# Optimization experiments

Measured on AMD Instinct MI355X. Metric: run time of the kernel, lower is better.

The kernel has to match this reference:

```python
import jax, jax.numpy as jnp
import numpy as np

B, T, C = 4, 2048, 1024
H = 16
D = C // H  # head_dim = 64


def setup_inputs() -> dict:
    key = jax.random.key(0)
    k1, k2, k3, k4, k5 = jax.random.split(key, 5)
    s = 0.02
    return {
        "x": jax.random.normal(k1, (B, T, C), dtype=jnp.float32),
        "W_qkv": jax.random.normal(k2, (C, 3 * C), dtype=jnp.float32) * s,
        "b_qkv": jax.random.normal(k3, (3 * C,), dtype=jnp.float32) * s,
        "W_o": jax.random.normal(k4, (C, C), dtype=jnp.float32) * s,
        "b_o": jax.random.normal(k5, (C,), dtype=jnp.float32) * s,
    }


def reference(x, W_qkv, b_qkv, W_o, b_o):
    b, t, c = x.shape
    scaling = D ** (-0.5)
    qkv = x @ W_qkv + b_qkv                      # [B,T,3C]
    q, k, v = jnp.split(qkv, 3, axis=-1)         # each [B,T,C]
    q = q.reshape(b, t, H, D).transpose(0, 2, 1, 3)  # [B,H,T,D]
    k = k.reshape(b, t, H, D).transpose(0, 2, 1, 3)
    v = v.reshape(b, t, H, D).transpose(0, 2, 1, 3)
    scores = jnp.einsum("bhqd,bhkd->bhqk", q, k) * scaling  # [B,H,T,T]
    mask = jnp.tril(jnp.ones((t, t), dtype=bool))            # causal
    scores = jnp.where(mask[None, None, :, :], scores, -jnp.inf)
    probs = jax.nn.softmax(scores, axis=-1)
    out = jnp.einsum("bhqk,bhkd->bhqd", probs, v)            # [B,H,T,D]
    out = out.transpose(0, 2, 1, 3).reshape(b, t, c)         # [B,T,C]
    return out @ W_o + b_o
```

## Files before the change

kernel.cpp:

```cpp
#include <hip/hip_runtime.h>
#include <hip/hip_bf16.h>

typedef unsigned short ushort_t;
typedef __attribute__((ext_vector_type(8))) short short8;
typedef __attribute__((ext_vector_type(4))) float floatx4;
typedef __attribute__((ext_vector_type(2))) unsigned uint2v;
typedef __attribute__((ext_vector_type(4))) unsigned uint4v;

#define B_ 4
#define T_ 2048
#define C_ 1024
#define H_ 16
#define D_ 64
#define BT_ (B_ * T_)
#define N3C (3 * C_)

#define KSC 0.18033688011112042f

__device__ __forceinline__ ushort_t f2bf(float f) {
    unsigned u = __float_as_uint(f);
    u += 0x7FFF + ((u >> 16) & 1);
    return (ushort_t)(u >> 16);
}
__device__ __forceinline__ unsigned pack2bf(float a, float b) {
    __hip_bfloat162 h = __float22bfloat162_rn(make_float2(a, b));
    return *(unsigned*)&h;
}

__device__ __forceinline__ void gload16(const ushort_t* g, ushort_t* l) {
    __builtin_amdgcn_global_load_lds((const __attribute__((address_space(1))) void*)g,
                                     (__attribute__((address_space(3))) void*)l, 16, 0, 0);
}

__global__ void convert_x_k(const float* __restrict__ xin, ushort_t* __restrict__ xb) {
    size_t i = ((size_t)blockIdx.x * 256 + threadIdx.x) * 8;
    const float* xf = xin + i;
    float4 a = *(const float4*)xf;
    float4 b = *(const float4*)(xf + 4);
    short8 o;
    o[0] = (short)f2bf(a.x); o[1] = (short)f2bf(a.y);
    o[2] = (short)f2bf(a.z); o[3] = (short)f2bf(a.w);
    o[4] = (short)f2bf(b.x); o[5] = (short)f2bf(b.y);
    o[6] = (short)f2bf(b.z); o[7] = (short)f2bf(b.w);
    *(short8*)&xb[i] = o;
}

__global__ void transpose_k(const float* __restrict__ in, ushort_t* __restrict__ out,
                            int R, int Nc) {
    __shared__ ushort_t t[32][33];
    int bc = blockIdx.x * 32;
    int br = blockIdx.y * 32;
    int lx = threadIdx.x & 31, ly = threadIdx.x >> 5;
#pragma unroll
    for (int i = 0; i < 4; ++i) {
        int r = ly + i * 8;
        t[r][lx] = f2bf(in[(size_t)(br + r) * Nc + bc + lx]);
    }
    __syncthreads();
#pragma unroll
    for (int i = 0; i < 4; ++i) {
        int r = ly + i * 8;
        out[(size_t)(bc + r) * R + br + lx] = t[lx][r];
    }
}

__global__ void vtrans_k(const ushort_t* __restrict__ in, ushort_t* __restrict__ out) {
    __shared__ ushort_t t[32][33];
    int bh = blockIdx.z;
    const ushort_t* I = in + (size_t)bh * T_ * D_;
    ushort_t* O = out + (size_t)bh * D_ * T_;
    int bt = blockIdx.x * 32, bd = blockIdx.y * 32;
    int lx = threadIdx.x & 31, ly = threadIdx.x >> 5;
#pragma unroll
    for (int i = 0; i < 4; ++i) {
        int r = ly + i * 8;
        t[r][lx] = I[(size_t)(bt + r) * D_ + bd + lx];
    }
    __syncthreads();
#pragma unroll
    for (int i = 0; i < 4; ++i) {
        int r = ly + i * 8;
        O[(size_t)(bd + r) * T_ + bt + lx] = t[lx][r];
    }
}

template <int MODE>
__launch_bounds__(256)
__global__ void gemm_bt(const ushort_t* __restrict__ A, const ushort_t* __restrict__ Bt,
                        const float* __restrict__ bias, float* __restrict__ Cout,
                        ushort_t* __restrict__ Qo, ushort_t* __restrict__ Ko,
                        ushort_t* __restrict__ Vo, int M, int N, int K) {
    __shared__ __align__(16) ushort_t Alds[128 * 32];
    __shared__ __align__(16) ushort_t Blds[128 * 32];
    int tid = threadIdx.x;
    int wave = tid >> 6, lane = tid & 63;
    int bm = blockIdx.x * 128, bn = blockIdx.y * 128;
    int wr = (wave >> 1) * 64, wc = (wave & 1) * 64;
    int lm = lane & 15, lk = (lane >> 4) * 8, lq = lane >> 4;

    floatx4 acc[4][4] = {};

    int srow = tid >> 2;
    int scol = (tid & 3) * 8;
    const ushort_t* Ab = A + (size_t)(bm + srow) * K + scol;
    const ushort_t* Bb = Bt + (size_t)(bn + srow) * K + scol;
    ushort_t* Al0 = &Alds[wave * 512];
    ushort_t* Al1 = &Alds[2048 + wave * 512];
    ushort_t* Bl0 = &Blds[wave * 512];
    ushort_t* Bl1 = &Blds[2048 + wave * 512];
    size_t rowskip = (size_t)64 * K;

    for (int k0 = 0; k0 < K; k0 += 32) {
        __syncthreads();
        gload16(Ab + k0, Al0);
        gload16(Ab + k0 + rowskip, Al1);
        gload16(Bb + k0, Bl0);
        gload16(Bb + k0 + rowskip, Bl1);
        __syncthreads();
        short8 af[4], bf[4];
#pragma unroll
        for (int i = 0; i < 4; ++i)
            af[i] = *(const short8*)&Alds[(wr + i * 16 + lm) * 32 + lk];
#pragma unroll
        for (int i = 0; i < 4; ++i)
            bf[i] = *(const short8*)&Blds[(wc + i * 16 + lm) * 32 + lk];
#pragma unroll
        for (int mi = 0; mi < 4; ++mi)
#pragma unroll
            for (int ni = 0; ni < 4; ++ni)
                acc[mi][ni] = __builtin_amdgcn_mfma_f32_16x16x32_bf16(
                    af[mi], bf[ni], acc[mi][ni], 0, 0, 0);
    }

#pragma unroll
    for (int mi = 0; mi < 4; ++mi) {
#pragma unroll
        for (int ni = 0; ni < 4; ++ni) {
            int col = bn + wc + ni * 16 + lm;
            float bv = bias[col];
#pragma unroll
            for (int r = 0; r < 4; ++r) {
                int row = bm + wr + mi * 16 + lq * 4 + r;
                float v = acc[mi][ni][r] + bv;
                if (MODE == 0) {
                    Cout[(size_t)row * N + col] = v;
                } else {
                    int b = row >> 11, t = row & (T_ - 1);
                    int which = col >> 10, c = col & (C_ - 1);
                    int h = c >> 6, d = c & 63;
                    int bh = b * H_ + h;
                    size_t idx = ((size_t)bh * T_ + t) * D_ + d;
                    if (which == 0)
                        Qo[idx] = f2bf(v * KSC);
                    else if (which == 1)
                        Ko[idx] = f2bf(v);
                    else
                        Vo[idx] = f2bf(v);
                }
            }
        }
    }
}

__launch_bounds__(256)
__global__ void attn_k(const ushort_t* __restrict__ Q, const ushort_t* __restrict__ K,
                       const ushort_t* __restrict__ Vt, ushort_t* __restrict__ O) {
    __shared__ __align__(16) ushort_t Klds[64 * 72];
    __shared__ __align__(16) ushort_t Vlds[64 * 72];

    int tid = threadIdx.x, wave = tid >> 6, lane = tid & 63;
    int id = blockIdx.x;
    int xcd = id & 7, j = id >> 3;
    int band = 31 - (j & 31);
    int bh = xcd + 8 * (j >> 5);
    int b = bh >> 4, h = bh & 15;
    int lm = lane & 15, lq = lane >> 4;

    const ushort_t* Qp = Q + (size_t)bh * T_ * D_;
    const ushort_t* Kp = K + (size_t)bh * T_ * D_;
    const ushort_t* Vp = Vt + (size_t)bh * D_ * T_;
    ushort_t* Ob = O + ((size_t)b * T_) * C_ + h * D_;

    int srow = tid >> 2, scol = (tid & 3) * 16;
    const ushort_t* Kg = Kp + (size_t)srow * D_ + scol;
    const ushort_t* Vg = Vp + (size_t)srow * T_ + scol;
    ushort_t* Kl = &Klds[srow * 72 + scol];
    ushort_t* Vl = &Vlds[srow * 72 + scol];

    short8 onesf = {};
    if (lm == 0) {
#pragma unroll
        for (int jj = 0; jj < 8; ++jj) onesf[jj] = (short)0x3F80;
    }

    int m0 = band * 64 + wave * 16;

    short8 qf0 = *(const short8*)&Qp[(size_t)(m0 + lm) * D_ + lq * 8];
    short8 qf1 = *(const short8*)&Qp[(size_t)(m0 + lm) * D_ + 32 + lq * 8];

    floatx4 oacc[5] = {};

    int ntw = band + 1;
    short8 kr0 = *(const short8*)Kg;
    short8 kr1 = *(const short8*)(Kg + 8);
    short8 vr0 = *(const short8*)Vg;
    short8 vr1 = *(const short8*)(Vg + 8);

    for (int it = 0; it < ntw; ++it) {
        __syncthreads();
        *(short8*)Kl = kr0;
        *(short8*)(Kl + 8) = kr1;
        *(short8*)Vl = vr0;
        *(short8*)(Vl + 8) = vr1;
        __syncthreads();

        if (it + 1 < ntw) {
            const ushort_t* kn = Kg + (size_t)(it + 1) * 64 * D_;
            const ushort_t* vn = Vg + (it + 1) * 64;
            kr0 = *(const short8*)kn;
            kr1 = *(const short8*)(kn + 8);
            vr0 = *(const short8*)vn;
            vr1 = *(const short8*)(vn + 8);
        }

        short8 kf[4][2], vf[4][2];
#pragma unroll
        for (int nt = 0; nt < 4; ++nt) {
            kf[nt][0] = *(const short8*)&Klds[(nt * 16 + lm) * 72 + lq * 8];
            kf[nt][1] = *(const short8*)&Klds[(nt * 16 + lm) * 72 + 32 + lq * 8];
        }

        floatx4 st[4] = {};
#pragma unroll
        for (int nt = 0; nt < 4; ++nt) {
            st[nt] = __builtin_amdgcn_mfma_f32_16x16x32_bf16(kf[nt][0], qf0, st[nt], 0, 0, 0);
            st[nt] = __builtin_amdgcn_mfma_f32_16x16x32_bf16(kf[nt][1], qf1, st[nt], 0, 0, 0);
        }

#pragma unroll
        for (int dt = 0; dt < 4; ++dt) {
            vf[dt][0] = *(const short8*)&Vlds[(dt * 16 + lm) * 72 + lq * 8];
            vf[dt][1] = *(const short8*)&Vlds[(dt * 16 + lm) * 72 + 32 + lq * 8];
        }

        int kv0 = it * 64;
        if (it == ntw - 1) {
            int mg = m0 + lm;
#pragma unroll
            for (int nt = 0; nt < 4; ++nt)
#pragma unroll
                for (int r = 0; r < 4; ++r) {
                    int kvg = kv0 + nt * 16 + lq * 4 + r;
                    if (kvg > mg) st[nt][r] = -__builtin_inff();
                }
        }

        unsigned e0 = pack2bf(exp2f(st[0][0]), exp2f(st[0][1]));
        unsigned e1 = pack2bf(exp2f(st[0][2]), exp2f(st[0][3]));
        unsigned e2 = pack2bf(exp2f(st[1][0]), exp2f(st[1][1]));
        unsigned e3 = pack2bf(exp2f(st[1][2]), exp2f(st[1][3]));
        unsigned e4 = pack2bf(exp2f(st[2][0]), exp2f(st[2][1]));
        unsigned e5 = pack2bf(exp2f(st[2][2]), exp2f(st[2][3]));
        unsigned e6 = pack2bf(exp2f(st[3][0]), exp2f(st[3][1]));
        unsigned e7 = pack2bf(exp2f(st[3][2]), exp2f(st[3][3]));

        uint2v ra = __builtin_amdgcn_permlane32_swap(e0, e2, false, false);
        uint2v wa = __builtin_amdgcn_permlane16_swap(ra[0], ra[1], false, false);
        uint2v rb = __builtin_amdgcn_permlane32_swap(e1, e3, false, false);
        uint2v wb = __builtin_amdgcn_permlane16_swap(rb[0], rb[1], false, false);
        uint2v rc = __builtin_amdgcn_permlane32_swap(e4, e6, false, false);
        uint2v wc = __builtin_amdgcn_permlane16_swap(rc[0], rc[1], false, false);
        uint2v rd = __builtin_amdgcn_permlane32_swap(e5, e7, false, false);
        uint2v wd = __builtin_amdgcn_permlane16_swap(rd[0], rd[1], false, false);

        short8 pb0 = __builtin_bit_cast(short8, (uint4v){wa[0], wb[0], wa[1], wb[1]});
        short8 pb1 = __builtin_bit_cast(short8, (uint4v){wc[0], wd[0], wc[1], wd[1]});

#pragma unroll
        for (int dt = 0; dt < 4; ++dt) {
            oacc[dt] = __builtin_amdgcn_mfma_f32_16x16x32_bf16(vf[dt][0], pb0, oacc[dt], 0, 0, 0);
            oacc[dt] = __builtin_amdgcn_mfma_f32_16x16x32_bf16(vf[dt][1], pb1, oacc[dt], 0, 0, 0);
        }
        oacc[4] = __builtin_amdgcn_mfma_f32_16x16x32_bf16(onesf, pb0, oacc[4], 0, 0, 0);
        oacc[4] = __builtin_amdgcn_mfma_f32_16x16x32_bf16(onesf, pb1, oacc[4], 0, 0, 0);
    }

    float li = __shfl(oacc[4][0], lm, 64);
    float inv = 1.0f / li;
    int tg = m0 + lm;
#pragma unroll
    for (int dt = 0; dt < 4; ++dt) {
        uint2 pk;
        pk.x = pack2bf(oacc[dt][0] * inv, oacc[dt][1] * inv);
        pk.y = pack2bf(oacc[dt][2] * inv, oacc[dt][3] * inv);
        *(uint2*)&Ob[(size_t)tg * C_ + dt * 16 + lq * 4] = pk;
    }
}

extern "C" void kernel_launch(void* const* d_in, const int* in_sizes, int n_in,
                              void* d_out, int out_size, void* d_ws, size_t ws_size,
                              hipStream_t stream) {
    const float* x    = (const float*)d_in[0];
    const float* Wqkv = (const float*)d_in[1];
    const float* bqkv = (const float*)d_in[2];
    const float* Wo   = (const float*)d_in[3];
    const float* bo   = (const float*)d_in[4];

    ushort_t* ws = (ushort_t*)d_ws;
    ushort_t* WqkvT = ws;
    ushort_t* WoT   = WqkvT + (size_t)N3C * C_;
    ushort_t* Xb    = WoT + (size_t)C_ * C_;
    ushort_t* Qs    = Xb + (size_t)BT_ * C_;
    ushort_t* Ks    = Qs + (size_t)BT_ * C_;
    ushort_t* Vs    = Ks + (size_t)BT_ * C_;
    ushort_t* Attn  = Vs + (size_t)BT_ * C_;

    convert_x_k<<<BT_ * C_ / (256 * 8), 256, 0, stream>>>(x, Xb);
    transpose_k<<<dim3(N3C / 32, C_ / 32), 256, 0, stream>>>(Wqkv, WqkvT, C_, N3C);
    transpose_k<<<dim3(C_ / 32, C_ / 32), 256, 0, stream>>>(Wo, WoT, C_, C_);
    gemm_bt<1><<<dim3(BT_ / 128, N3C / 128), 256, 0, stream>>>(
        Xb, WqkvT, bqkv, nullptr, Qs, Ks, Attn, BT_, N3C, C_);
    vtrans_k<<<dim3(T_ / 32, D_ / 32, B_ * H_), 256, 0, stream>>>(Attn, Vs);
    attn_k<<<2048, 256, 0, stream>>>(Qs, Ks, Vs, Attn);
    gemm_bt<0><<<dim3(BT_ / 128, C_ / 128), 256, 0, stream>>>(
        Attn, WoT, bo, (float*)d_out, nullptr, nullptr, nullptr, BT_, C_, C_);
}
```

Measured before the change: 290.4 us.

## Double-buffer K/V tiles in LDS with direct global-to-LDS loads and XOR swizzle

The attention kernel now stages K and V tiles through a two-slot LDS buffer filled by direct global-to-LDS loads (gload16), replacing the register-staged copy. The padded 72-stride layout becomes an XOR-swizzled 64-stride layout to avoid bank conflicts. This removes one of the two barriers per iteration and the register round-trip. It also swaps exp2f for the raw hardware exp2 builtin, which drops the range handling the library call performs. It relies on gload16 being defined elsewhere and doubles the LDS footprint.

```diff
diff --git a/kernel.cpp b/kernel.cpp
--- a/kernel.cpp
+++ b/kernel.cpp
@@ -165,8 +165,7 @@
 __launch_bounds__(256)
 __global__ void attn_k(const ushort_t* __restrict__ Q, const ushort_t* __restrict__ K,
                        const ushort_t* __restrict__ Vt, ushort_t* __restrict__ O) {
-    __shared__ __align__(16) ushort_t Klds[64 * 72];
-    __shared__ __align__(16) ushort_t Vlds[64 * 72];
+    __shared__ __align__(16) ushort_t KV[2][2][64 * 64];
 
     int tid = threadIdx.x, wave = tid >> 6, lane = tid & 63;
     int id = blockIdx.x;
@@ -174,18 +173,19 @@
     int band = 31 - (j & 31);
     int bh = xcd + 8 * (j >> 5);
     int b = bh >> 4, h = bh & 15;
-    int lm = lane & 15, lq = lane >> 4;
+    int lm = lane & 15, lq = lane >> 4, m7 = lane & 7;
 
     const ushort_t* Qp = Q + (size_t)bh * T_ * D_;
     const ushort_t* Kp = K + (size_t)bh * T_ * D_;
     const ushort_t* Vp = Vt + (size_t)bh * D_ * T_;
     ushort_t* Ob = O + ((size_t)b * T_) * C_ + h * D_;
 
-    int srow = tid >> 2, scol = (tid & 3) * 16;
-    const ushort_t* Kg = Kp + (size_t)srow * D_ + scol;
-    const ushort_t* Vg = Vp + (size_t)srow * T_ + scol;
-    ushort_t* Kl = &Klds[srow * 72 + scol];
-    ushort_t* Vl = &Vlds[srow * 72 + scol];
+    int sr = lane >> 3;
+    int sc = (lane & 7) ^ sr;
+    const ushort_t* Kst = Kp + (size_t)(wave * 16 + sr) * D_ + sc * 8;
+    const ushort_t* Vst = Vp + (size_t)(wave * 16 + sr) * T_ + sc * 8;
+    int lds0 = (wave * 2 + 0) * 512;
+    int lds1 = (wave * 2 + 1) * 512;
 
     short8 onesf = {};
     if (lm == 0) {
@@ -201,33 +201,30 @@
     floatx4 oacc[5] = {};
 
     int ntw = band + 1;
-    short8 kr0 = *(const short8*)Kg;
-    short8 kr1 = *(const short8*)(Kg + 8);
-    short8 vr0 = *(const short8*)Vg;
-    short8 vr1 = *(const short8*)(Vg + 8);
-
+
+    gload16(Kst, &KV[0][0][lds0]);
+    gload16(Kst + (size_t)8 * D_, &KV[0][0][lds1]);
+    gload16(Vst, &KV[0][1][lds0]);
+    gload16(Vst + (size_t)8 * T_, &KV[0][1][lds1]);
+    __syncthreads();
+
+    int cur = 0;
     for (int it = 0; it < ntw; ++it) {
-        __syncthreads();
-        *(short8*)Kl = kr0;
-        *(short8*)(Kl + 8) = kr1;
-        *(short8*)Vl = vr0;
-        *(short8*)(Vl + 8) = vr1;
-        __syncthreads();
-
         if (it + 1 < ntw) {
-            const ushort_t* kn = Kg + (size_t)(it + 1) * 64 * D_;
-            const ushort_t* vn = Vg + (it + 1) * 64;
-            kr0 = *(const short8*)kn;
-            kr1 = *(const short8*)(kn + 8);
-            vr0 = *(const short8*)vn;
-            vr1 = *(const short8*)(vn + 8);
-        }
+            size_t kv0n = (size_t)(it + 1) * 64;
+            gload16(Kst + kv0n * D_, &KV[cur ^ 1][0][lds0]);
+            gload16(Kst + kv0n * D_ + 8 * D_, &KV[cur ^ 1][0][lds1]);
+            gload16(Vst + kv0n, &KV[cur ^ 1][1][lds0]);
+            gload16(Vst + kv0n + 8 * T_, &KV[cur ^ 1][1][lds1]);
+        }
+        const ushort_t* Kb = &KV[cur][0][0];
+        const ushort_t* Vb = &KV[cur][1][0];
 
         short8 kf[4][2], vf[4][2];
 #pragma unroll
         for (int nt = 0; nt < 4; ++nt) {
-            kf[nt][0] = *(const short8*)&Klds[(nt * 16 + lm) * 72 + lq * 8];
-            kf[nt][1] = *(const short8*)&Klds[(nt * 16 + lm) * 72 + 32 + lq * 8];
+            kf[nt][0] = *(const short8*)&Kb[(nt * 16 + lm) * 64 + ((lq ^ m7) * 8)];
+            kf[nt][1] = *(const short8*)&Kb[(nt * 16 + lm) * 64 + (((lq + 4) ^ m7) * 8)];
         }
 
         floatx4 st[4] = {};
@@ -239,8 +236,8 @@
 
 #pragma unroll
         for (int dt = 0; dt < 4; ++dt) {
-            vf[dt][0] = *(const short8*)&Vlds[(dt * 16 + lm) * 72 + lq * 8];
-            vf[dt][1] = *(const short8*)&Vlds[(dt * 16 + lm) * 72 + 32 + lq * 8];
+            vf[dt][0] = *(const short8*)&Vb[(dt * 16 + lm) * 64 + ((lq ^ m7) * 8)];
+            vf[dt][1] = *(const short8*)&Vb[(dt * 16 + lm) * 64 + (((lq + 4) ^ m7) * 8)];
         }
 
         int kv0 = it * 64;
@@ -255,14 +252,14 @@
                 }
         }
 
-        unsigned e0 = pack2bf(exp2f(st[0][0]), exp2f(st[0][1]));
-        unsigned e1 = pack2bf(exp2f(st[0][2]), exp2f(st[0][3]));
-        unsigned e2 = pack2bf(exp2f(st[1][0]), exp2f(st[1][1]));
-        unsigned e3 = pack2bf(exp2f(st[1][2]), exp2f(st[1][3]));
-        unsigned e4 = pack2bf(exp2f(st[2][0]), exp2f(st[2][1]));
-        unsigned e5 = pack2bf(exp2f(st[2][2]), exp2f(st[2][3]));
-        unsigned e6 = pack2bf(exp2f(st[3][0]), exp2f(st[3][1]));
-        unsigned e7 = pack2bf(exp2f(st[3][2]), exp2f(st[3][3]));
+        unsigned e0 = pack2bf(__builtin_amdgcn_exp2f(st[0][0]), __builtin_amdgcn_exp2f(st[0][1]));
+        unsigned e1 = pack2bf(__builtin_amdgcn_exp2f(st[0][2]), __builtin_amdgcn_exp2f(st[0][3]));
+        unsigned e2 = pack2bf(__builtin_amdgcn_exp2f(st[1][0]), __builtin_amdgcn_exp2f(st[1][1]));
+        unsigned e3 = pack2bf(__builtin_amdgcn_exp2f(st[1][2]), __builtin_amdgcn_exp2f(st[1][3]));
+        unsigned e4 = pack2bf(__builtin_amdgcn_exp2f(st[2][0]), __builtin_amdgcn_exp2f(st[2][1]));
+        unsigned e5 = pack2bf(__builtin_amdgcn_exp2f(st[2][2]), __builtin_amdgcn_exp2f(st[2][3]));
+        unsigned e6 = pack2bf(__builtin_amdgcn_exp2f(st[3][0]), __builtin_amdgcn_exp2f(st[3][1]));
+        unsigned e7 = pack2bf(__builtin_amdgcn_exp2f(st[3][2]), __builtin_amdgcn_exp2f(st[3][3]));
 
         uint2v ra = __builtin_amdgcn_permlane32_swap(e0, e2, false, false);
         uint2v wa = __builtin_amdgcn_permlane16_swap(ra[0], ra[1], false, false);
@@ -283,6 +280,9 @@
         }
         oacc[4] = __builtin_amdgcn_mfma_f32_16x16x32_bf16(onesf, pb0, oacc[4], 0, 0, 0);
         oacc[4] = __builtin_amdgcn_mfma_f32_16x16x32_bf16(onesf, pb1, oacc[4], 0, 0, 0);
+
+        __syncthreads();
+        cur ^= 1;
     }
 
     float li = __shfl(oacc[4][0], lm, 64);
```

Result: faster. 278.9 us (-4.0%).
